# Kernel tuning notes

Measured on AMD Instinct MI355X. Metric: run time of the kernel, lower is better.

Reference implementation:

```python
import jax, jax.numpy as jnp
import numpy as np
import math

D_HEAD = 64  # scaling uses sqrt(d_head), NOT sqrt of full projection dim (faithful to source)

def setup_inputs() -> dict:
    key = jax.random.key(0)
    ks = jax.random.split(key, 9)
    B, S, D = 4, 2048, 1024
    s = 0.02
    return {
        "x": jax.random.normal(ks[0], (B, S, D), dtype=jnp.float32),
        "Wq": jax.random.normal(ks[1], (D, D), dtype=jnp.float32) * s,
        "bq": jax.random.normal(ks[2], (D,), dtype=jnp.float32) * s,
        "Wk": jax.random.normal(ks[3], (D, D), dtype=jnp.float32) * s,
        "bk": jax.random.normal(ks[4], (D,), dtype=jnp.float32) * s,
        "Wv": jax.random.normal(ks[5], (D, D), dtype=jnp.float32) * s,
        "bv": jax.random.normal(ks[6], (D,), dtype=jnp.float32) * s,
        "Wo": jax.random.normal(ks[7], (D, D), dtype=jnp.float32) * s,
        "bo": jax.random.normal(ks[8], (D,), dtype=jnp.float32) * s,
    }

def reference(x, Wq, bq, Wk, bk, Wv, bv, Wo, bo):
    # Q/K/V projections: [B,S,D] @ [D,D] + b
    Q = jnp.einsum('bsd,de->bse', x, Wq) + bq
    K = jnp.einsum('bsd,de->bse', x, Wk) + bk
    V = jnp.einsum('bsd,de->bse', x, Wv) + bv
    # NOTE: source does bmm over the FULL projected dim (no head split),
    # scaled by sqrt(d_head) only.
    scores = jnp.einsum('bqd,bkd->bqk', Q, K) / math.sqrt(D_HEAD)  # [B,S,S]
    S_len = scores.shape[-1]
    causal = jnp.tril(jnp.ones((S_len, S_len), dtype=bool))
    scores = jnp.where(causal, scores, -jnp.inf)
    weights = jax.nn.softmax(scores, axis=-1)
    attn_out = jnp.einsum('bqk,bkd->bqd', weights, V)
    return jnp.einsum('bsd,de->bse', attn_out, Wo) + bo
```

## Files before the change

### kernel.cpp

```cpp
#include <hip/hip_runtime.h>
#include <stdint.h>

typedef _Float16 f16;
typedef __attribute__((ext_vector_type(8))) _Float16 f16x8;
typedef __attribute__((ext_vector_type(4))) _Float16 f16x4;
typedef __attribute__((ext_vector_type(4))) float f32x4;

#define BK 32

typedef __attribute__((address_space(3))) uint32_t lds_u32;
typedef const __attribute__((address_space(1))) uint32_t glb_u32;

__device__ __forceinline__ void gload_lds16(const void* g, void* l) {
    __builtin_amdgcn_global_load_lds((glb_u32*)g, (lds_u32*)l, 16, 0, 0);
}

template<int OUT_MODE, int CAUSAL, int TM, int TN>
__global__ __launch_bounds__(256, 2)
void gemm_bt(const f16* __restrict__ A, const f16* __restrict__ B,
             const float* __restrict__ bias, const float* __restrict__ bias2,
             void* __restrict__ Cv, void* __restrict__ C2,
             int M, int N, int K,
             long long sAb, long long sBb, long long sCb, float scale)
{
    constexpr int IM = TM / 32;
    constexpr int JN = TN / 32;

    int mtile, n0;
    if (CAUSAL == 1) {
        int rem = (int)blockIdx.x, mi = 0;
        while (rem > mi) { rem -= mi + 1; ++mi; }
        mtile = mi;
        n0 = rem * TN;
    } else {
        mtile = blockIdx.y;
        n0 = blockIdx.x * TN;
    }

    const int tid  = threadIdx.x;
    const int wave = tid >> 6;
    const int lane = tid & 63;
    const long long bz = blockIdx.z;
    A += bz * sAb;
    B += bz * sBb;

    __shared__ f16 As[TM * BK];
    __shared__ f16 Bs[TN * BK];

    const int srow  = lane >> 2;
    const int scolS = (((lane & 3) ^ ((srow >> 1) & 3))) * 8;
    const int fr    = lane & 15;
    const int fkS   = (((lane >> 4) ^ ((fr >> 1) & 3))) * 8;

    const int wm = (wave >> 1) * (TM / 2);
    const int wn = (wave & 1) * (TN / 2);

    const int npass = (CAUSAL == 2) ? 2 : 1;
    for (int pass = 0; pass < npass; ++pass) {
        const int mt = (CAUSAL == 2 && pass == 1) ? (M / TM - 1 - mtile) : mtile;
        const int m0 = mt * TM;
        const int Kend = (CAUSAL == 2) ? (m0 + TM) : K;

        f32x4 acc[IM][JN] = {};

        for (int k0 = 0; k0 < Kend; k0 += BK) {
            #pragma unroll
            for (int gg = 0; gg < TM / 64; ++gg) {
                const int g = wave * (TM / 64) + gg;
                gload_lds16(A + (long long)(m0 + g * 16 + srow) * K + (k0 + scolS),
                            &As[g * 512]);
            }
            #pragma unroll
            for (int gg = 0; gg < TN / 64; ++gg) {
                const int g = wave * (TN / 64) + gg;
                gload_lds16(B + (long long)(n0 + g * 16 + srow) * K + (k0 + scolS),
                            &Bs[g * 512]);
            }
            __syncthreads();

            f16x8 af[IM], bf[JN];
            #pragma unroll
            for (int i = 0; i < IM; ++i)
                af[i] = *(const f16x8*)&As[(wm + i * 16 + fr) * BK + fkS];
            #pragma unroll
            for (int j = 0; j < JN; ++j)
                bf[j] = *(const f16x8*)&Bs[(wn + j * 16 + fr) * BK + fkS];

            #pragma unroll
            for (int i = 0; i < IM; ++i)
                #pragma unroll
                for (int j = 0; j < JN; ++j)
                    acc[i][j] = __builtin_amdgcn_mfma_f32_16x16x32_f16(af[i], bf[j], acc[i][j], 0, 0, 0);
            __syncthreads();
        }

        const int cn = lane & 15;
        const int cm = (lane >> 4) * 4;
        #pragma unroll
        for (int j = 0; j < JN; ++j) {
            const int gn = n0 + wn + j * 16 + cn;
            #pragma unroll
            for (int i = 0; i < IM; ++i) {
                const int gm = m0 + wm + i * 16 + cm;
                if (OUT_MODE == 0) {
                    const float bv = bias ? bias[gn] : 0.f;
                    float* C = (float*)Cv + bz * sCb;
                    #pragma unroll
                    for (int r = 0; r < 4; ++r)
                        C[(long long)(gm + r) * N + gn] = acc[i][j][r] * scale + bv;
                } else if (OUT_MODE == 1) {
                    const float bv = bias ? bias[(long long)bz * N + gn] : 0.f;
                    f16* C = (f16*)Cv + bz * sCb;
                    #pragma unroll
                    for (int r = 0; r < 4; ++r)
                        C[(long long)(gm + r) * N + gn] = (f16)(acc[i][j][r] * scale + bv);
                } else {
                    const int sel = gn >> 10;
                    const int nn  = gn & 1023;
                    if (sel == 0) {
                        f16* C = (f16*)Cv;
                        #pragma unroll
                        for (int r = 0; r < 4; ++r)
                            C[(long long)(gm + r) * 1024 + nn] = (f16)acc[i][j][r];
                    } else {
                        const float bb = bias2[nn];
                        f16* C = (f16*)C2;
                        const int b = gm >> 11, s = gm & 2047;
                        f16x4 pk;
                        #pragma unroll
                        for (int r = 0; r < 4; ++r)
                            pk[r] = (f16)(acc[i][j][r] + bb);
                        *(f16x4*)&C[(long long)b * 2097152 + (long long)nn * 2048 + s] = pk;
                    }
                }
            }
        }
        if (CAUSAL == 2) __syncthreads();
    }
}

__global__ __launch_bounds__(256)
void cast_to_f16(const float* __restrict__ in, f16* __restrict__ out, int n)
{
    const int i = (blockIdx.x * 256 + threadIdx.x) * 4;
    if (i < n) {
        const float4 v = *(const float4*)&in[i];
        f16x4 o;
        o[0] = (f16)v.x; o[1] = (f16)v.y; o[2] = (f16)v.z; o[3] = (f16)v.w;
        *(f16x4*)&out[i] = o;
    }
}

__global__ void transpose_cast(const float* __restrict__ in, f16* __restrict__ out,
                               int rows, int cols)
{
    __shared__ f16 tile[32][33];
    const int bx = blockIdx.x * 32;
    const int by = blockIdx.y * 32;
    const int tx = threadIdx.x;
    const int ty = threadIdx.y;
    #pragma unroll
    for (int i = 0; i < 32; i += 8)
        tile[ty + i][tx] = (f16)in[(long long)(by + ty + i) * cols + (bx + tx)];
    __syncthreads();
    #pragma unroll
    for (int i = 0; i < 32; i += 8)
        out[(long long)(bx + ty + i) * rows + (by + tx)] = tile[tx][ty + i];
}

__global__ __launch_bounds__(256)
void bias_vo(const float* __restrict__ bv, const float* __restrict__ Wo,
             float* __restrict__ bvo)
{
    const int e0 = blockIdx.x * 64;
    const int wave = threadIdx.x >> 6, lane = threadIdx.x & 63;
    float acc = 0.f;
    for (int i = 0; i < 256; ++i) {
        const int k = wave * 256 + i;
        acc += bv[k] * Wo[(long long)k * 1024 + e0 + lane];
    }
    __shared__ float red[4][64];
    red[wave][lane] = acc;
    __syncthreads();
    if (wave == 0)
        bvo[e0 + lane] = red[0][lane] + red[1][lane] + red[2][lane] + red[3][lane];
}

__global__ __launch_bounds__(256)
void wk_bq(const float* __restrict__ Wk, const float* __restrict__ bq,
           float* __restrict__ w)
{
    const int row = blockIdx.x * 4 + (threadIdx.x >> 6);
    const int lane = threadIdx.x & 63;
    const float* src = Wk + (long long)row * 1024;
    float a = 0.f;
    #pragma unroll
    for (int t = 0; t < 16; ++t) a += src[lane + 64 * t] * bq[lane + 64 * t];
    #pragma unroll
    for (int o = 32; o > 0; o >>= 1) a += __shfl_down(a, o);
    if (lane == 0) w[row] = a * 0.125f;
}

__global__ __launch_bounds__(256)
void cvec(const f16* __restrict__ xb, const float* __restrict__ w,
          float* __restrict__ c)
{
    const int row = blockIdx.x * 4 + (threadIdx.x >> 6);
    const int lane = threadIdx.x & 63;
    const f16* src = xb + (long long)row * 1024;
    float a = 0.f;
    #pragma unroll
    for (int t = 0; t < 16; ++t) a += (float)src[lane + 64 * t] * w[lane + 64 * t];
    #pragma unroll
    for (int o = 32; o > 0; o >>= 1) a += __shfl_down(a, o);
    if (lane == 0) c[row] = a;
}

__global__ __launch_bounds__(256)
void softmax_causal(const f16* __restrict__ Sc, f16* __restrict__ P, int S)
{
    const long long row = blockIdx.x;
    const int q = (int)(row % S);
    const f16* src = Sc + row * S;
    f16* dst = P + row * S;
    const int t = threadIdx.x;
    __shared__ float redm[4], reds[4];

    const f16x8 vv = *(const f16x8*)&src[t * 8];
    float v[8];
    float mx = -3.0e38f;
    #pragma unroll
    for (int i = 0; i < 8; ++i) {
        const int k = t * 8 + i;
        v[i] = (float)vv[i];
        if (k <= q) mx = fmaxf(mx, v[i]);
    }
    #pragma unroll
    for (int o = 32; o > 0; o >>= 1) mx = fmaxf(mx, __shfl_down(mx, o));
    if ((t & 63) == 0) redm[t >> 6] = mx;
    __syncthreads();
    mx = fmaxf(fmaxf(redm[0], redm[1]), fmaxf(redm[2], redm[3]));

    float sum = 0.f;
    #pragma unroll
    for (int i = 0; i < 8; ++i) {
        const int k = t * 8 + i;
        v[i] = (k <= q) ? __expf(v[i] - mx) : 0.f;
        sum += v[i];
    }
    #pragma unroll
    for (int o = 32; o > 0; o >>= 1) sum += __shfl_down(sum, o);
    if ((t & 63) == 0) reds[t >> 6] = sum;
    __syncthreads();
    sum = reds[0] + reds[1] + reds[2] + reds[3];
    const float inv = 1.f / sum;
    f16x8 ov;
    #pragma unroll
    for (int i = 0; i < 8; ++i) ov[i] = (f16)(v[i] * inv);
    *(f16x8*)&dst[t * 8] = ov;
}

extern "C" void kernel_launch(void* const* d_in, const int* in_sizes, int n_in,
                              void* d_out, int out_size, void* d_ws, size_t ws_size,
                              hipStream_t stream)
{
    const float* x  = (const float*)d_in[0];
    const float* Wq = (const float*)d_in[1];
    const float* bq = (const float*)d_in[2];
    const float* Wk = (const float*)d_in[3];
    const float* Wv = (const float*)d_in[5];
    const float* bv = (const float*)d_in[6];
    const float* Wo = (const float*)d_in[7];
    const float* bo = (const float*)d_in[8];
    float* out = (float*)d_out;

    const int B = 4, S = 2048, D = 1024;
    const long long SD  = (long long)S * D;
    const long long SS  = (long long)S * S;
    const long long BSD = (long long)B * SD;
    const int MS = B * S;

    char* p = (char*)d_ws;
    f16*   xb    = (f16*)p;  p += BSD * 2;
    f16*   Wqf   = (f16*)p;  p += (long long)D * D * 2;
    f16*   Wkf   = (f16*)p;  p += (long long)D * D * 2;
    f16*   Wvf   = (f16*)p;  p += (long long)D * D * 2;
    f16*   Wot   = (f16*)p;  p += (long long)D * D * 2;
    f16*   Wcat2 = (f16*)p;  p += 2LL * D * D * 2;
    float* bvo   = (float*)p; p += D * 4;
    float* wv    = (float*)p; p += D * 4;
    float* cbias = (float*)p; p += (long long)MS * 4;
    f16*   Qh    = (f16*)p;  p += BSD * 2;
    f16*   Vt    = (f16*)p;  p += BSD * 2;
    f16*   Sc    = (f16*)p;  p += (long long)B * SS * 2;
    f16*   Pb    = (f16*)p;  p += (long long)B * SS * 2;

    dim3 blk(256);

    cast_to_f16<<<dim3((unsigned)(BSD / 4 / 256)), blk, 0, stream>>>(x, xb, (int)BSD);
    cast_to_f16<<<dim3((unsigned)(D * D / 4 / 256)), blk, 0, stream>>>(Wq, Wqf, D * D);
    cast_to_f16<<<dim3((unsigned)(D * D / 4 / 256)), blk, 0, stream>>>(Wk, Wkf, D * D);
    cast_to_f16<<<dim3((unsigned)(D * D / 4 / 256)), blk, 0, stream>>>(Wv, Wvf, D * D);
    dim3 tb(32, 8), tg(D / 32, D / 32);
    transpose_cast<<<tg, tb, 0, stream>>>(Wo, Wot, D, D);
    bias_vo<<<dim3(16), blk, 0, stream>>>(bv, Wo, bvo);
    wk_bq<<<dim3(D / 4), blk, 0, stream>>>(Wk, bq, wv);
    cvec<<<dim3(MS / 4), blk, 0, stream>>>(xb, wv, cbias);

    dim3 gw(D / 64, D / 64, 1);
    gemm_bt<1, 0, 64, 64><<<gw, blk, 0, stream>>>(Wkf, Wqf, nullptr, nullptr,
                                                  Wcat2, nullptr,
                                                  D, D, D, 0, 0, 0, 1.f);
    gemm_bt<1, 0, 64, 64><<<gw, blk, 0, stream>>>(Wot, Wvf, nullptr, nullptr,
                                                  Wcat2 + (long long)D * D, nullptr,
                                                  D, D, D, 0, 0, 0, 1.f);

    dim3 gproj(2 * D / 128, MS / 128, 1);
    gemm_bt<3, 0, 128, 128><<<gproj, blk, 0, stream>>>(xb, Wcat2, nullptr, bvo,
                                                       Qh, Vt,
                                                       MS, 2 * D, D, 0, 0, 0, 1.f);

    dim3 gsc(136, 1, B);
    gemm_bt<1, 1, 128, 128><<<gsc, blk, 0, stream>>>(Qh, xb, cbias, nullptr,
                                                     Sc, nullptr,
                                                     S, S, D, SD, SD, SS, 0.125f);

    softmax_causal<<<dim3((unsigned)(B * S)), blk, 0, stream>>>(Sc, Pb, S);

    dim3 gpv(D / 64, S / 128 / 2, B);
    gemm_bt<0, 2, 128, 64><<<gpv, blk, 0, stream>>>(Pb, Vt, bo, nullptr,
                                                    out, nullptr,
                                                    S, D, S, SS, SD, SD, 1.f);
}
```

Measured before the change: 305.1 us.

## Merge prep kernels into one launch and fuse weight GEMMs with cvec

Result: faster. 276.6 us (-9.3%).

```diff
diff --git a/kernel.cpp b/kernel.cpp
--- a/kernel.cpp
+++ b/kernel.cpp
@@ -16,31 +16,32 @@
 }
 
 template<int OUT_MODE, int CAUSAL, int TM, int TN>
-__global__ __launch_bounds__(256, 2)
-void gemm_bt(const f16* __restrict__ A, const f16* __restrict__ B,
-             const float* __restrict__ bias, const float* __restrict__ bias2,
-             void* __restrict__ Cv, void* __restrict__ C2,
-             int M, int N, int K,
-             long long sAb, long long sBb, long long sCb, float scale)
+__device__ __forceinline__
+void gemm_body(const f16* __restrict__ A, const f16* __restrict__ B,
+               const float* __restrict__ bias, const float* __restrict__ bias2,
+               void* __restrict__ Cv, void* __restrict__ C2,
+               int M, int N, int K,
+               long long sAb, long long sBb, long long sCb, float scale,
+               int bx, int by, int bzi)
 {
     constexpr int IM = TM / 32;
     constexpr int JN = TN / 32;
 
     int mtile, n0;
     if (CAUSAL == 1) {
-        int rem = (int)blockIdx.x, mi = 0;
+        int rem = bx, mi = 0;
         while (rem > mi) { rem -= mi + 1; ++mi; }
         mtile = mi;
         n0 = rem * TN;
     } else {
-        mtile = blockIdx.y;
-        n0 = blockIdx.x * TN;
+        mtile = by;
+        n0 = bx * TN;
     }
 
     const int tid  = threadIdx.x;
     const int wave = tid >> 6;
     const int lane = tid & 63;
-    const long long bz = blockIdx.z;
+    const long long bz = bzi;
     A += bz * sAb;
     B += bz * sBb;
 
@@ -139,81 +140,122 @@
     }
 }
 
+template<int OUT_MODE, int CAUSAL, int TM, int TN>
+__global__ __launch_bounds__(256, 2)
+void gemm_bt(const f16* __restrict__ A, const f16* __restrict__ B,
+             const float* __restrict__ bias, const float* __restrict__ bias2,
+             void* __restrict__ Cv, void* __restrict__ C2,
+             int M, int N, int K,
+             long long sAb, long long sBb, long long sCb, float scale)
+{
+    gemm_body<OUT_MODE, CAUSAL, TM, TN>(A, B, bias, bias2, Cv, C2, M, N, K,
+                                        sAb, sBb, sCb, scale,
+                                        blockIdx.x, blockIdx.y, blockIdx.z);
+}
+
 __global__ __launch_bounds__(256)
-void cast_to_f16(const float* __restrict__ in, f16* __restrict__ out, int n)
-{
-    const int i = (blockIdx.x * 256 + threadIdx.x) * 4;
-    if (i < n) {
-        const float4 v = *(const float4*)&in[i];
-        f16x4 o;
-        o[0] = (f16)v.x; o[1] = (f16)v.y; o[2] = (f16)v.z; o[3] = (f16)v.w;
-        *(f16x4*)&out[i] = o;
-    }
-}
-
-__global__ void transpose_cast(const float* __restrict__ in, f16* __restrict__ out,
-                               int rows, int cols)
+void prep(const float* __restrict__ x,  const float* __restrict__ Wq,
+          const float* __restrict__ bq, const float* __restrict__ Wk,
+          const float* __restrict__ Wv, const float* __restrict__ bv,
+          const float* __restrict__ Wo,
+          f16* __restrict__ xb,  f16* __restrict__ Wqf, f16* __restrict__ Wkf,
+          f16* __restrict__ Wvf, f16* __restrict__ Wot,
+          float* __restrict__ bvo, float* __restrict__ wvec)
 {
     __shared__ f16 tile[32][33];
-    const int bx = blockIdx.x * 32;
-    const int by = blockIdx.y * 32;
-    const int tx = threadIdx.x;
-    const int ty = threadIdx.y;
-    #pragma unroll
-    for (int i = 0; i < 32; i += 8)
-        tile[ty + i][tx] = (f16)in[(long long)(by + ty + i) * cols + (bx + tx)];
-    __syncthreads();
-    #pragma unroll
-    for (int i = 0; i < 32; i += 8)
-        out[(long long)(bx + ty + i) * rows + (by + tx)] = tile[tx][ty + i];
-}
-
-__global__ __launch_bounds__(256)
-void bias_vo(const float* __restrict__ bv, const float* __restrict__ Wo,
-             float* __restrict__ bvo)
-{
-    const int e0 = blockIdx.x * 64;
-    const int wave = threadIdx.x >> 6, lane = threadIdx.x & 63;
-    float acc = 0.f;
-    for (int i = 0; i < 256; ++i) {
-        const int k = wave * 256 + i;
-        acc += bv[k] * Wo[(long long)k * 1024 + e0 + lane];
-    }
     __shared__ float red[4][64];
-    red[wave][lane] = acc;
-    __syncthreads();
-    if (wave == 0)
-        bvo[e0 + lane] = red[0][lane] + red[1][lane] + red[2][lane] + red[3][lane];
-}
-
-__global__ __launch_bounds__(256)
-void wk_bq(const float* __restrict__ Wk, const float* __restrict__ bq,
-           float* __restrict__ w)
-{
-    const int row = blockIdx.x * 4 + (threadIdx.x >> 6);
-    const int lane = threadIdx.x & 63;
-    const float* src = Wk + (long long)row * 1024;
-    float a = 0.f;
-    #pragma unroll
-    for (int t = 0; t < 16; ++t) a += src[lane + 64 * t] * bq[lane + 64 * t];
-    #pragma unroll
-    for (int o = 32; o > 0; o >>= 1) a += __shfl_down(a, o);
-    if (lane == 0) w[row] = a * 0.125f;
-}
-
-__global__ __launch_bounds__(256)
-void cvec(const f16* __restrict__ xb, const float* __restrict__ w,
-          float* __restrict__ c)
-{
-    const int row = blockIdx.x * 4 + (threadIdx.x >> 6);
-    const int lane = threadIdx.x & 63;
-    const f16* src = xb + (long long)row * 1024;
-    float a = 0.f;
-    #pragma unroll
-    for (int t = 0; t < 16; ++t) a += (float)src[lane + 64 * t] * w[lane + 64 * t];
-    #pragma unroll
-    for (int o = 32; o > 0; o >>= 1) a += __shfl_down(a, o);
-    if (lane == 0) c[row] = a;
+    const int t = threadIdx.x;
+    int id = blockIdx.x;
+
+    if (id < 8192) {
+        const int i = (id * 256 + t) * 4;
+        const float4 v = *(const float4*)&x[i];
+        f16x4 o; o[0]=(f16)v.x; o[1]=(f16)v.y; o[2]=(f16)v.z; o[3]=(f16)v.w;
+        *(f16x4*)&xb[i] = o;
+        return;
+    }
+    id -= 8192;
+    if (id < 3072) {
+        const float* src = (id < 1024) ? Wq : (id < 2048) ? Wk : Wv;
+        f16* dst = (id < 1024) ? Wqf : (id < 2048) ? Wkf : Wvf;
+        const int i = ((id & 1023) * 256 + t) * 4;
+        const float4 v = *(const float4*)&src[i];
+        f16x4 o; o[0]=(f16)v.x; o[1]=(f16)v.y; o[2]=(f16)v.z; o[3]=(f16)v.w;
+        *(f16x4*)&dst[i] = o;
+        return;
+    }
+    id -= 3072;
+    if (id < 1024) {
+        const int bx = (id & 31) * 32, by = (id >> 5) * 32;
+        const int tx = t & 31, ty = t >> 5;
+        #pragma unroll
+        for (int i = 0; i < 32; i += 8)
+            tile[ty + i][tx] = (f16)Wo[(long long)(by + ty + i) * 1024 + (bx + tx)];
+        __syncthreads();
+        #pragma unroll
+        for (int i = 0; i < 32; i += 8)
+            Wot[(long long)(bx + ty + i) * 1024 + (by + tx)] = tile[tx][ty + i];
+        return;
+    }
+    id -= 1024;
+    if (id < 16) {
+        const int e0 = id * 64;
+        const int wave = t >> 6, lane = t & 63;
+        float acc = 0.f;
+        for (int i = 0; i < 256; ++i) {
+            const int k = wave * 256 + i;
+            acc += bv[k] * Wo[(long long)k * 1024 + e0 + lane];
+        }
+        red[wave][lane] = acc;
+        __syncthreads();
+        if (wave == 0)
+            bvo[e0 + lane] = red[0][lane] + red[1][lane] + red[2][lane] + red[3][lane];
+        return;
+    }
+    id -= 16;
+    {
+        const int row = id * 4 + (t >> 6);
+        const int lane = t & 63;
+        const float* src = Wk + (long long)row * 1024;
+        float a = 0.f;
+        #pragma unroll
+        for (int tt = 0; tt < 16; ++tt) a += src[lane + 64 * tt] * bq[lane + 64 * tt];
+        #pragma unroll
+        for (int o = 32; o > 0; o >>= 1) a += __shfl_down(a, o);
+        if (lane == 0) wvec[row] = a * 0.125f;
+    }
+}
+
+__global__ __launch_bounds__(256, 2)
+void dual_weights_cvec(const f16* __restrict__ Wkf, const f16* __restrict__ Wqf,
+                       const f16* __restrict__ Wot, const f16* __restrict__ Wvf,
+                       f16* __restrict__ Wcat2,
+                       const f16* __restrict__ xb, const float* __restrict__ wvec,
+                       float* __restrict__ cbias)
+{
+    if (blockIdx.z == 2) {
+        const int flat = blockIdx.y * 16 + blockIdx.x;
+        const int wave = threadIdx.x >> 6, lane = threadIdx.x & 63;
+        #pragma unroll
+        for (int rr = 0; rr < 8; ++rr) {
+            const int row = (flat * 4 + wave) * 8 + rr;
+            const f16* src = xb + (long long)row * 1024;
+            float a = 0.f;
+            #pragma unroll
+            for (int tt = 0; tt < 16; ++tt)
+                a += (float)src[lane + 64 * tt] * wvec[lane + 64 * tt];
+            #pragma unroll
+            for (int o = 32; o > 0; o >>= 1) a += __shfl_down(a, o);
+            if (lane == 0) cbias[row] = a;
+        }
+        return;
+    }
+    const f16* Ax = (blockIdx.z == 0) ? Wkf : Wot;
+    const f16* Bx = (blockIdx.z == 0) ? Wqf : Wvf;
+    f16* Cx = Wcat2 + (long long)blockIdx.z * 1024 * 1024;
+    gemm_body<1, 0, 64, 64>(Ax, Bx, nullptr, nullptr, Cx, nullptr,
+                            1024, 1024, 1024, 0, 0, 0, 1.f,
+                            blockIdx.x, blockIdx.y, 0);
 }
 
 __global__ __launch_bounds__(256)
@@ -226,7 +268,8 @@
     const int t = threadIdx.x;
     __shared__ float redm[4], reds[4];
 
-    const f16x8 vv = *(const f16x8*)&src[t * 8];
+    f16x8 vv = {};
+    if (t * 8 <= q) vv = *(const f16x8*)&src[t * 8];
     float v[8];
     float mx = -3.0e38f;
     #pragma unroll
@@ -288,7 +331,7 @@
     f16*   Wot   = (f16*)p;  p += (long long)D * D * 2;
     f16*   Wcat2 = (f16*)p;  p += 2LL * D * D * 2;
     float* bvo   = (float*)p; p += D * 4;
-    float* wv    = (float*)p; p += D * 4;
+    float* wvec  = (float*)p; p += D * 4;
     float* cbias = (float*)p; p += (long long)MS * 4;
     f16*   Qh    = (f16*)p;  p += BSD * 2;
     f16*   Vt    = (f16*)p;  p += BSD * 2;
@@ -297,23 +340,11 @@
 
     dim3 blk(256);
 
-    cast_to_f16<<<dim3((unsigned)(BSD / 4 / 256)), blk, 0, stream>>>(x, xb, (int)BSD);
-    cast_to_f16<<<dim3((unsigned)(D * D / 4 / 256)), blk, 0, stream>>>(Wq, Wqf, D * D);
-    cast_to_f16<<<dim3((unsigned)(D * D / 4 / 256)), blk, 0, stream>>>(Wk, Wkf, D * D);
-    cast_to_f16<<<dim3((unsigned)(D * D / 4 / 256)), blk, 0, stream>>>(Wv, Wvf, D * D);
-    dim3 tb(32, 8), tg(D / 32, D / 32);
-    transpose_cast<<<tg, tb, 0, stream>>>(Wo, Wot, D, D);
-    bias_vo<<<dim3(16), blk, 0, stream>>>(bv, Wo, bvo);
-    wk_bq<<<dim3(D / 4), blk, 0, stream>>>(Wk, bq, wv);
-    cvec<<<dim3(MS / 4), blk, 0, stream>>>(xb, wv, cbias);
-
-    dim3 gw(D / 64, D / 64, 1);
-    gemm_bt<1, 0, 64, 64><<<gw, blk, 0, stream>>>(Wkf, Wqf, nullptr, nullptr,
-                                                  Wcat2, nullptr,
-                                                  D, D, D, 0, 0, 0, 1.f);
-    gemm_bt<1, 0, 64, 64><<<gw, blk, 0, stream>>>(Wot, Wvf, nullptr, nullptr,
-                                                  Wcat2 + (long long)D * D, nullptr,
-                                                  D, D, D, 0, 0, 0, 1.f);
+    prep<<<dim3(12560), blk, 0, stream>>>(x, Wq, bq, Wk, Wv, bv, Wo,
+                                          xb, Wqf, Wkf, Wvf, Wot, bvo, wvec);
+
+    dual_weights_cvec<<<dim3(16, 16, 3), blk, 0, stream>>>(Wkf, Wqf, Wot, Wvf,
+                                                           Wcat2, xb, wvec, cbias);
 
     dim3 gproj(2 * D / 128, MS / 128, 1);
     gemm_bt<3, 0, 128, 128><<<gproj, blk, 0, stream>>>(xb, Wcat2, nullptr, bvo,
```
